# Kernel optimization log

Measured on AMD Instinct MI355X. Metric: run time of the kernel, lower is better.

The kernel has to match this reference:

```python
import jax, jax.numpy as jnp
import numpy as np

EPS = 1e-5

def _ln(x, g):
    # LayerNorm over the 3H gate dimension, scale-only (haste LayerNormGRU style)
    m = jnp.mean(x, axis=-1, keepdims=True)
    v = jnp.var(x, axis=-1, keepdims=True)
    return (x - m) * jax.lax.rsqrt(v + EPS) * g

def _gru_layer(x, h0, W, R, bx, br, gw, gr):
    # x: [B,T,D], h0: [B,H]; returns ([B,T,H], [B,H])
    H = R.shape[0]
    wx = _ln(jnp.einsum('btd,dk->btk', x, W), gw)  # [B,T,3H], LN precomputable (no h dep)

    def step(h, wx_t):
        rh = _ln(h @ R, gr)  # [B,3H]
        z = jax.nn.sigmoid(wx_t[:, :H] + bx[:H] + rh[:, :H] + br[:H])
        r = jax.nn.sigmoid(wx_t[:, H:2*H] + bx[H:2*H] + rh[:, H:2*H] + br[H:2*H])
        g = jnp.tanh(wx_t[:, 2*H:] + bx[2*H:] + r * (rh[:, 2*H:] + br[2*H:]))
        h_new = z * h + (1.0 - z) * g
        return h_new, h_new

    h_last, hs = jax.lax.scan(step, h0, jnp.swapaxes(wx, 0, 1))  # scan over T
    return jnp.swapaxes(hs, 0, 1), h_last

def setup_inputs() -> dict:
    key = jax.random.key(0)
    ks = jax.random.split(key, 8)
    B, T, IN, H, OUT, L = 32, 512, 128, 1024, 80, 3
    s_in = 1.0 / np.sqrt(IN)
    s_h = 1.0 / np.sqrt(H)
    return {
        'x': jax.random.normal(ks[0], (B, T, IN), jnp.float32),
        'W0': jax.random.normal(ks[1], (IN, 3 * H), jnp.float32) * s_in,
        'R0': jax.random.normal(ks[2], (H, 3 * H), jnp.float32) * s_h,
        'bx0': jnp.zeros((3 * H,), jnp.float32),
        'br0': jnp.zeros((3 * H,), jnp.float32),
        'gw0': jnp.ones((3 * H,), jnp.float32),
        'gr0': jnp.ones((3 * H,), jnp.float32),
        'Wk': jax.random.normal(ks[3], (L - 1, H, 3 * H), jnp.float32) * s_h,
        'Rk': jax.random.normal(ks[4], (L - 1, H, 3 * H), jnp.float32) * s_h,
        'bxk': jnp.zeros((L - 1, 3 * H), jnp.float32),
        'brk': jnp.zeros((L - 1, 3 * H), jnp.float32),
        'gwk': jnp.ones((L - 1, 3 * H), jnp.float32),
        'grk': jnp.ones((L - 1, 3 * H), jnp.float32),
        'Wlin': jax.random.normal(ks[5], (H, OUT), jnp.float32) * s_h,
        'blin': jnp.zeros((OUT,), jnp.float32),
    }

def reference(x, W0, R0, bx0, br0, gw0, gr0, Wk, Rk, bxk, brk, gwk, grk, Wlin, blin):
    B = x.shape[0]
    H = R0.shape[0]
    h0 = jnp.zeros((B, H), x.dtype)
    h, hs = _gru_layer(x, h0, W0, R0, bx0, br0, gw0, gr0)
    for i in range(Wk.shape[0]):  # stacked layers share state chain (state=h_s)
        h, hs = _gru_layer(h, hs, Wk[i], Rk[i], bxk[i], brk[i], gwk[i], grk[i])
    return jnp.tanh(h @ Wlin + blin)
```

## Files before the change

### kernel.cpp

```cpp
#include <hip/hip_runtime.h>


typedef float    f32x4 __attribute__((ext_vector_type(4)));
typedef _Float16 f16x8 __attribute__((ext_vector_type(8)));

#define HH      1024
#define TT      512
#define BBATCH  32
#define H3      3072
#define MROWS   16384
#define NBLK_R  128
#define HPB     8
#define COLS    24
#define LN_EPS  1e-5f

#define OFF_CTRL   0u
#define OFF_PSTAT  8192u
#define OFF_H      40960u
#define OFF_HF     106496u
#define CTRL_BYTES 237568u
#define OFF_WLB    327680u
#define OFF_WB     524288u
#define OFF_XBF    (8ull<<20)
#define OFF_WX     (16ull<<20)
#define OFF_HSA    (112ull<<20)
#define OFF_HSB    (144ull<<20)

#define ALOAD(p)    __hip_atomic_load((p),  __ATOMIC_RELAXED, __HIP_MEMORY_SCOPE_AGENT)
#define ASTORE(p,v) __hip_atomic_store((p), (v), __ATOMIC_RELAXED, __HIP_MEMORY_SCOPE_AGENT)
#define AADD(p)     __hip_atomic_fetch_add((p), 1u, __ATOMIC_RELAXED, __HIP_MEMORY_SCOPE_AGENT)

__device__ __forceinline__ f16x8 ldg_h16(const _Float16* p) {
  f16x8 r;
  asm volatile("global_load_dwordx4 %0, %1, off sc0 sc1" : "=v"(r) : "v"(p));
  return r;
}
__device__ __forceinline__ f32x4 ldg_f32x4(const float* p) {
  f32x4 r;
  asm volatile("global_load_dwordx4 %0, %1, off sc0 sc1" : "=v"(r) : "v"(p));
  return r;
}

__device__ __forceinline__ float sigf(float x) {
  return __builtin_amdgcn_rcpf(1.f + __expf(-x));
}
__device__ __forceinline__ float tanhfast(float x) {
  const float e2 = __expf(2.f * x);
  return 1.f - 2.f * __builtin_amdgcn_rcpf(e2 + 1.f);
}

__global__ __launch_bounds__(256, 1) void k_init(
    const float* __restrict__ x, _Float16* __restrict__ xb,
    const float* __restrict__ Wlin, _Float16* __restrict__ Wlb)
{
  const size_t stride = (size_t)gridDim.x * 256;
  for (size_t i = (size_t)blockIdx.x * 256 + threadIdx.x; i < (size_t)MROWS * 128; i += stride)
    xb[i] = (_Float16)x[i];
  for (size_t i = (size_t)blockIdx.x * 256 + threadIdx.x; i < 80u * 1024u; i += stride) {
    const size_t n = i >> 10, k = i & 1023u;
    Wlb[i] = (_Float16)Wlin[k * 80 + n];
  }
}

__global__ __launch_bounds__(256, 1) void k_convW(
    const float* __restrict__ W, _Float16* __restrict__ Wb, const int K)
{
  const int n = blockIdx.x;
  for (int k = threadIdx.x; k < K; k += 256)
    Wb[(size_t)n * K + k] = (_Float16)W[(size_t)k * H3 + n];
}

__global__ __launch_bounds__(256, 1) void k_gemm(
    const _Float16* __restrict__ A,
    const _Float16* __restrict__ Bw,
    _Float16* __restrict__ Cw,
    const int K)
{
  __shared__ _Float16 Bs[64][40];
  const int tid = threadIdx.x;
  const int lane = tid & 63, wv = tid >> 6;
  const int l15 = lane & 15, quad = lane >> 4;
  const int tilem = blockIdx.x / 48, tilen = blockIdx.x % 48;
  const int mbase = tilem * 64 + wv * 16;
  const size_t nbase = (size_t)tilen * 64;
  f32x4 acc[4] = {{0.f,0.f,0.f,0.f},{0.f,0.f,0.f,0.f},{0.f,0.f,0.f,0.f},{0.f,0.f,0.f,0.f}};
  const _Float16* arow = A + (size_t)(mbase + l15) * K + quad * 8;
  const int sn = tid >> 2, sk = (tid & 3) * 8;
  const _Float16* bsrc = Bw + (nbase + sn) * K + sk;
  for (int kc = 0; kc < K; kc += 32) {
    __syncthreads();
    *(f16x8*)(&Bs[sn][sk]) = *(const f16x8*)(bsrc + kc);
    __syncthreads();
    const f16x8 af = *(const f16x8*)(arow + kc);
#pragma unroll
    for (int nt = 0; nt < 4; ++nt) {
      const f16x8 bv = *(const f16x8*)(&Bs[nt * 16 + l15][quad * 8]);
      acc[nt] = __builtin_amdgcn_mfma_f32_16x16x32_f16(af, bv, acc[nt], 0, 0, 0);
    }
  }
#pragma unroll
  for (int nt = 0; nt < 4; ++nt)
#pragma unroll
    for (int j = 0; j < 4; ++j)
      Cw[(size_t)(mbase + quad * 4 + j) * H3 + nbase + nt * 16 + l15] = (_Float16)acc[nt][j];
}

__global__ __launch_bounds__(256, 1) void k_ln(
    _Float16* __restrict__ wxp, const float* __restrict__ gw)
{
  const int wv = threadIdx.x >> 6, lane = threadIdx.x & 63;
  const size_t row = (size_t)blockIdx.x * 4 + wv;
  _Float16* p = wxp + row * H3 + lane * 8;
  float vals[48];
  float s = 0.f, q = 0.f;
#pragma unroll
  for (int c = 0; c < 6; ++c) {
    const f16x8 v = *(const f16x8*)(p + c * 512);
#pragma unroll
    for (int j = 0; j < 8; ++j) {
      const float f = (float)v[j];
      vals[c * 8 + j] = f; s += f; q += f * f;
    }
  }
#pragma unroll
  for (int m = 1; m < 64; m <<= 1) { s += __shfl_xor(s, m); q += __shfl_xor(q, m); }
  const float mean = s * (1.f / H3);
  const float var  = q * (1.f / H3) - mean * mean;
  const float inv  = rsqrtf(var + LN_EPS);
#pragma unroll
  for (int c = 0; c < 6; ++c) {
    f16x8 o;
#pragma unroll
    for (int j = 0; j < 8; ++j)
      o[j] = (_Float16)((vals[c * 8 + j] - mean) * inv * gw[c * 512 + lane * 8 + j]);
    *(f16x8*)(p + c * 512) = o;
  }
}

__global__ __launch_bounds__(256, 1) void k_recur(
    const float* __restrict__ R, const float* __restrict__ bx,
    const float* __restrict__ br, const float* __restrict__ gr,
    const _Float16* __restrict__ wx,
    _Float16* __restrict__ hs_out,
    unsigned* __restrict__ hglob,
    float* __restrict__ hf32,
    float* __restrict__ pstat,
    unsigned* __restrict__ ctrl,
    const unsigned abase,
    const unsigned hbase)
{
  const int tid = threadIdx.x;
  const int blk = blockIdx.x;
  unsigned* cntA = ctrl;
  unsigned* cntB = ctrl + 1024;

  __shared__ _Float16 Rs[COLS][HH + 8];
  __shared__ float rhp[2][BBATCH][27];
  __shared__ float statb[BBATCH][2];
  __shared__ float pred[16][68];

  const int lane = tid & 63;
  const int wv   = tid >> 6;
  const int mh   = wv >> 1;
  const int kh   = wv & 1;
  const int l15  = lane & 15;
  const int quad = lane >> 4;
  const int kb   = kh * 512;
  const int lineB = ((blk & 7) * 4 + wv) * 32;

  for (int n = 0; n < COLS; ++n) {
    const int gc = (n >> 3) * HH + blk * HPB + (n & 7);
    for (int k = tid; k < HH; k += 256)
      Rs[n][k] = (_Float16)R[(size_t)k * H3 + gc];
  }

  const int b_row = tid >> 3;
  const int jj    = tid & 7;
  const int gi    = blk * HPB + jj;
  const float bxz = bx[gi], bxr = bx[HH + gi], bxg = bx[2 * HH + gi];
  const float brz = br[gi], brr = br[HH + gi], brg = br[2 * HH + gi];
  const float grz = gr[gi], grr = gr[HH + gi], grg = gr[2 * HH + gi];
  float hloc = hf32[b_row * HH + gi];

  {
    union { _Float16 f; unsigned short s; } hc; hc.f = (_Float16)hloc;
    const unsigned short mybits = hc.s;
    const unsigned short pbits  = (unsigned short)__shfl_xor((int)mybits, 1);
    if ((jj & 1) == 0) {
      const unsigned w = (unsigned)mybits | ((unsigned)pbits << 16);
      ASTORE(&hglob[blk * 128 + b_row * 4 + (jj >> 1)], w);
    }
  }
  asm volatile("s_waitcnt vmcnt(0)" ::: "memory");
  if (lane == 0) AADD(&cntB[lineB]);

  const _Float16* hread = (const _Float16*)hglob;
  const _Float16* hrow  = hread + (size_t)(kh * 64 + quad) * 256
                                + (size_t)(mh * 16 + l15) * 8;
  const int n1 = 16 + (l15 & 7);

  for (int t = 0; t < TT; ++t) {
    const _Float16* wrow = wx + (size_t)(b_row * TT + t) * H3;
    const float wz = (float)wrow[gi];
    const float wr = (float)wrow[HH + gi];
    const float wg = (float)wrow[2 * HH + gi];

    if (tid < 32) {
      const unsigned* p = cntB + tid * 32;
      const unsigned tgt = 16u * (hbase + (unsigned)t + 1u);
      int spins = 0;
      while (ALOAD(p) < tgt) { if (++spins > (1 << 24)) break; }
    }
    __syncthreads();

    f16x8 af[16];
#pragma unroll
    for (int ks = 0; ks < 16; ++ks)
      af[ks] = ldg_h16(hrow + ks * 1024);
    asm volatile("s_waitcnt vmcnt(0)" ::: "memory");
    f32x4 acc0 = {0.f,0.f,0.f,0.f}, acc1 = {0.f,0.f,0.f,0.f};
#pragma unroll
    for (int ks = 0; ks < 16; ++ks) {
      const f16x8 b0 = *(const f16x8*)(&Rs[l15][kb + ks * 32 + quad * 8]);
      acc0 = __builtin_amdgcn_mfma_f32_16x16x32_f16(af[ks], b0, acc0, 0, 0, 0);
      const f16x8 b1 = *(const f16x8*)(&Rs[n1][kb + ks * 32 + quad * 8]);
      acc1 = __builtin_amdgcn_mfma_f32_16x16x32_f16(af[ks], b1, acc1, 0, 0, 0);
    }
#pragma unroll
    for (int j = 0; j < 4; ++j) {
      rhp[kh][mh * 16 + quad * 4 + j][l15] = acc0[j];
      if (l15 < 8) rhp[kh][mh * 16 + quad * 4 + j][16 + l15] = acc1[j];
    }
    __syncthreads();

    const float rz = rhp[0][b_row][jj]      + rhp[1][b_row][jj];
    const float rr = rhp[0][b_row][8 + jj]  + rhp[1][b_row][8 + jj];
    const float rg = rhp[0][b_row][16 + jj] + rhp[1][b_row][16 + jj];
    {
      float s = rz + rr + rg;
      float q = rz * rz + rr * rr + rg * rg;
      s += __shfl_xor(s, 1); q += __shfl_xor(q, 1);
      s += __shfl_xor(s, 2); q += __shfl_xor(q, 2);
      s += __shfl_xor(s, 4); q += __shfl_xor(q, 4);
      if (jj == 0) { statb[b_row][0] = s; statb[b_row][1] = q; }
    }
    __syncthreads();
    if (tid < 64) ASTORE(&pstat[blk * 64 + tid], statb[tid >> 1][tid & 1]);
    asm volatile("s_waitcnt vmcnt(0)" ::: "memory");
    if (tid == 0) AADD(&cntA[(blk & 31) * 32]);

    if (tid < 32) {
      const unsigned* p = cntA + tid * 32;
      const unsigned tgt = 4u * (abase + (unsigned)t + 1u);
      int spins = 0;
      while (ALOAD(p) < tgt) { if (++spins > (1 << 24)) break; }
    }
    __syncthreads();

    {
      const int prow0 = tid >> 4;
      const int pcol  = (tid & 15) * 4;
      f32x4 pv0 = ldg_f32x4(pstat + (size_t)(prow0      ) * 64 + pcol);
      f32x4 pv1 = ldg_f32x4(pstat + (size_t)(prow0 +  16) * 64 + pcol);
      f32x4 pv2 = ldg_f32x4(pstat + (size_t)(prow0 +  32) * 64 + pcol);
      f32x4 pv3 = ldg_f32x4(pstat + (size_t)(prow0 +  48) * 64 + pcol);
      f32x4 pv4 = ldg_f32x4(pstat + (size_t)(prow0 +  64) * 64 + pcol);
      f32x4 pv5 = ldg_f32x4(pstat + (size_t)(prow0 +  80) * 64 + pcol);
      f32x4 pv6 = ldg_f32x4(pstat + (size_t)(prow0 +  96) * 64 + pcol);
      f32x4 pv7 = ldg_f32x4(pstat + (size_t)(prow0 + 112) * 64 + pcol);
      asm volatile("s_waitcnt vmcnt(0)" ::: "memory");
      const f32x4 pa = ((pv0 + pv1) + (pv2 + pv3)) + ((pv4 + pv5) + (pv6 + pv7));
      *(f32x4*)(&pred[prow0][pcol]) = pa;
    }
    __syncthreads();
    float sfs = 0.f, sfq = 0.f;
#pragma unroll
    for (int g = 0; g < 16; ++g) {
      sfs += pred[g][2 * b_row];
      sfq += pred[g][2 * b_row + 1];
    }

    const float mean = sfs * (1.f / H3);
    const float var  = sfq * (1.f / H3) - mean * mean;
    const float inv  = __frsqrt_rn(var + LN_EPS);
    const float rzn = (rz - mean) * inv * grz;
    const float rrn = (rr - mean) * inv * grr;
    const float rgn = (rg - mean) * inv * grg;
    const float zg    = sigf(wz + bxz + rzn + brz);
    const float rgate = sigf(wr + bxr + rrn + brr);
    const float gg    = tanhfast(wg + bxg + rgate * (rgn + brg));
    const float hn = zg * hloc + (1.f - zg) * gg;
    hloc = hn;
    union { _Float16 f; unsigned short s; } hc; hc.f = (_Float16)hn;
    const unsigned short mybits = hc.s;
    const unsigned short pbits  = (unsigned short)__shfl_xor((int)mybits, 1);
    if ((jj & 1) == 0) {
      const unsigned w = (unsigned)mybits | ((unsigned)pbits << 16);
      ASTORE(&hglob[blk * 128 + b_row * 4 + (jj >> 1)], w);
    }
    hs_out[(size_t)(b_row * TT + t) * HH + gi] = hc.f;
    asm volatile("s_waitcnt vmcnt(0)" ::: "memory");
    if (lane == 0) AADD(&cntB[lineB]);
  }
  hf32[b_row * HH + gi] = hloc;
}

__global__ __launch_bounds__(256, 1) void k_proj(
    const _Float16* __restrict__ hs,
    const _Float16* __restrict__ Wlb,
    const float* __restrict__ blin,
    float* __restrict__ out)
{
  const int tid = threadIdx.x, lane = tid & 63, wv = tid >> 6;
  const int l15 = lane & 15, quad = lane >> 4;
  const int mbase = blockIdx.x * 64 + wv * 16;
  f32x4 acc[5] = {{0.f,0.f,0.f,0.f},{0.f,0.f,0.f,0.f},{0.f,0.f,0.f,0.f},
                  {0.f,0.f,0.f,0.f},{0.f,0.f,0.f,0.f}};
  const _Float16* arow = hs + (size_t)(mbase + l15) * HH + quad * 8;
  for (int kc = 0; kc < HH; kc += 32) {
    const f16x8 af = *(const f16x8*)(arow + kc);
#pragma unroll
    for (int nt = 0; nt < 5; ++nt) {
      const f16x8 bv = *(const f16x8*)(Wlb + (size_t)(nt * 16 + l15) * HH + kc + quad * 8);
      acc[nt] = __builtin_amdgcn_mfma_f32_16x16x32_f16(af, bv, acc[nt], 0, 0, 0);
    }
  }
#pragma unroll
  for (int nt = 0; nt < 5; ++nt)
#pragma unroll
    for (int j = 0; j < 4; ++j) {
      const int col = nt * 16 + l15;
      out[(size_t)(mbase + quad * 4 + j) * 80 + col] = tanhf(acc[nt][j] + blin[col]);
    }
}

extern "C" void kernel_launch(void* const* d_in, const int* in_sizes, int n_in,
                              void* d_out, int out_size, void* d_ws, size_t ws_size,
                              hipStream_t stream)
{
  const float* x    = (const float*)d_in[0];
  const float* W0   = (const float*)d_in[1];
  const float* R0   = (const float*)d_in[2];
  const float* bx0  = (const float*)d_in[3];
  const float* br0  = (const float*)d_in[4];
  const float* gw0  = (const float*)d_in[5];
  const float* gr0  = (const float*)d_in[6];
  const float* Wk   = (const float*)d_in[7];
  const float* Rk   = (const float*)d_in[8];
  const float* bxk  = (const float*)d_in[9];
  const float* brk  = (const float*)d_in[10];
  const float* gwk  = (const float*)d_in[11];
  const float* grk  = (const float*)d_in[12];
  const float* Wlin = (const float*)d_in[13];
  const float* blin = (const float*)d_in[14];

  char* ws = (char*)d_ws;
  unsigned*  ctrl   = (unsigned*)(ws + OFF_CTRL);
  float*     pstat  = (float*)(ws + OFF_PSTAT);
  unsigned*  hglob  = (unsigned*)(ws + OFF_H);
  float*     hf32   = (float*)(ws + OFF_HF);
  _Float16*  Wlb    = (_Float16*)(ws + OFF_WLB);
  _Float16*  Wb     = (_Float16*)(ws + OFF_WB);
  _Float16*  xb     = (_Float16*)(ws + OFF_XBF);
  _Float16*  wx     = (_Float16*)(ws + OFF_WX);
  _Float16*  hsA    = (_Float16*)(ws + OFF_HSA);
  _Float16*  hsB    = (_Float16*)(ws + OFF_HSB);

  hipMemsetAsync(d_ws, 0, CTRL_BYTES, stream);

  k_init<<<2048, 256, 0, stream>>>(x, xb, Wlin, Wlb);

  for (int l = 0; l < 3; ++l) {
    const int K = l ? HH : 128;
    const float* Wl  = l ? (Wk  + (size_t)(l - 1) * HH * H3) : W0;
    const float* Rl  = l ? (Rk  + (size_t)(l - 1) * HH * H3) : R0;
    const float* bxl = l ? (bxk + (size_t)(l - 1) * H3) : bx0;
    const float* brl = l ? (brk + (size_t)(l - 1) * H3) : br0;
    const float* gwl = l ? (gwk + (size_t)(l - 1) * H3) : gw0;
    const float* grl = l ? (grk + (size_t)(l - 1) * H3) : gr0;
    const _Float16* Ain = (l == 0) ? xb : ((l == 1) ? hsA : hsB);
    _Float16* hs_out = (l == 1) ? hsB : hsA;

    k_convW<<<H3, 256, 0, stream>>>(Wl, Wb, K);
    k_gemm<<<12288, 256, 0, stream>>>(Ain, Wb, wx, K);
    k_ln<<<4096, 256, 0, stream>>>(wx, gwl);
    k_recur<<<NBLK_R, 256, 0, stream>>>(Rl, bxl, brl, grl, wx, hs_out,
                                        hglob, hf32, pstat, ctrl,
                                        (unsigned)l * (unsigned)TT,
                                        (unsigned)l * (TT + 1u));
  }
  k_proj<<<256, 256, 0, stream>>>(hsA, Wlb, blin, (float*)d_out);
}
```

Baseline: 10.68 ms.

## Replace counter barrier for LN stats with tagged data polling

Removes the cntA atomic-counter barrier used to exchange per-block LayerNorm partial sums across the 128 recurrent blocks. Each block now writes its sum and sum-of-squares together with a timestep tag in one 16-byte store, and readers spin on the tag embedded in the data itself. This saves a store-wait-atomic-poll round trip on every timestep. It relies on 16-byte stores being seen whole and on float tags staying exact, and all 256 threads now poll global memory.

```diff
diff --git a/kernel.cpp b/kernel.cpp
--- a/kernel.cpp
+++ b/kernel.cpp
@@ -15,10 +15,10 @@
 #define LN_EPS  1e-5f
 
 #define OFF_CTRL   0u
-#define OFF_PSTAT  8192u
-#define OFF_H      40960u
-#define OFF_HF     106496u
-#define CTRL_BYTES 237568u
+#define OFF_PST    4096u
+#define OFF_H      69632u
+#define OFF_HF     135168u
+#define CTRL_BYTES 266240u
 #define OFF_WLB    327680u
 #define OFF_WB     524288u
 #define OFF_XBF    (8ull<<20)
@@ -39,6 +39,9 @@
   f32x4 r;
   asm volatile("global_load_dwordx4 %0, %1, off sc0 sc1" : "=v"(r) : "v"(p));
   return r;
+}
+__device__ __forceinline__ void stg_f32x4(float* p, f32x4 v) {
+  asm volatile("global_store_dwordx4 %0, %1, off sc0 sc1" :: "v"(p), "v"(v) : "memory");
 }
 
 __device__ __forceinline__ float sigf(float x) {
@@ -144,20 +147,20 @@
     _Float16* __restrict__ hs_out,
     unsigned* __restrict__ hglob,
     float* __restrict__ hf32,
-    float* __restrict__ pstat,
+    float* __restrict__ pst,
     unsigned* __restrict__ ctrl,
     const unsigned abase,
     const unsigned hbase)
 {
   const int tid = threadIdx.x;
   const int blk = blockIdx.x;
-  unsigned* cntA = ctrl;
-  unsigned* cntB = ctrl + 1024;
+  unsigned* cntB = ctrl;
 
   __shared__ _Float16 Rs[COLS][HH + 8];
   __shared__ float rhp[2][BBATCH][27];
   __shared__ float statb[BBATCH][2];
-  __shared__ float pred[16][68];
+  __shared__ float predS[8][33];
+  __shared__ float predQ[8][33];
 
   const int lane = tid & 63;
   const int wv   = tid >> 6;
@@ -198,8 +201,12 @@
   const _Float16* hrow  = hread + (size_t)(kh * 64 + quad) * 256
                                 + (size_t)(mh * 16 + l15) * 8;
   const int n1 = 16 + (l15 & 7);
+  const int grp = tid >> 5;
+  const int rr  = tid & 31;
+  const float* gbase = pst + ((size_t)(grp * 16) * 32 + rr) * 4;
 
   for (int t = 0; t < TT; ++t) {
+    const float tagf = (float)(abase + (unsigned)t + 1u);
     const _Float16* wrow = wx + (size_t)(b_row * TT + t) * H3;
     const float wz = (float)wrow[gi];
     const float wr = (float)wrow[HH + gi];
@@ -234,57 +241,57 @@
     __syncthreads();
 
     const float rz = rhp[0][b_row][jj]      + rhp[1][b_row][jj];
-    const float rr = rhp[0][b_row][8 + jj]  + rhp[1][b_row][8 + jj];
+    const float rr2 = rhp[0][b_row][8 + jj]  + rhp[1][b_row][8 + jj];
     const float rg = rhp[0][b_row][16 + jj] + rhp[1][b_row][16 + jj];
     {
-      float s = rz + rr + rg;
-      float q = rz * rz + rr * rr + rg * rg;
+      float s = rz + rr2 + rg;
+      float q = rz * rz + rr2 * rr2 + rg * rg;
       s += __shfl_xor(s, 1); q += __shfl_xor(q, 1);
       s += __shfl_xor(s, 2); q += __shfl_xor(q, 2);
       s += __shfl_xor(s, 4); q += __shfl_xor(q, 4);
       if (jj == 0) { statb[b_row][0] = s; statb[b_row][1] = q; }
     }
     __syncthreads();
-    if (tid < 64) ASTORE(&pstat[blk * 64 + tid], statb[tid >> 1][tid & 1]);
-    asm volatile("s_waitcnt vmcnt(0)" ::: "memory");
-    if (tid == 0) AADD(&cntA[(blk & 31) * 32]);
 
     if (tid < 32) {
-      const unsigned* p = cntA + tid * 32;
-      const unsigned tgt = 4u * (abase + (unsigned)t + 1u);
-      int spins = 0;
-      while (ALOAD(p) < tgt) { if (++spins > (1 << 24)) break; }
-    }
-    __syncthreads();
+      f32x4 pv;
+      pv[0] = statb[tid][0]; pv[1] = tagf;
+      pv[2] = statb[tid][1]; pv[3] = tagf;
+      stg_f32x4(pst + ((size_t)blk * 32 + tid) * 4, pv);
+    }
 
     {
-      const int prow0 = tid >> 4;
-      const int pcol  = (tid & 15) * 4;
-      f32x4 pv0 = ldg_f32x4(pstat + (size_t)(prow0      ) * 64 + pcol);
-      f32x4 pv1 = ldg_f32x4(pstat + (size_t)(prow0 +  16) * 64 + pcol);
-      f32x4 pv2 = ldg_f32x4(pstat + (size_t)(prow0 +  32) * 64 + pcol);
-      f32x4 pv3 = ldg_f32x4(pstat + (size_t)(prow0 +  48) * 64 + pcol);
-      f32x4 pv4 = ldg_f32x4(pstat + (size_t)(prow0 +  64) * 64 + pcol);
-      f32x4 pv5 = ldg_f32x4(pstat + (size_t)(prow0 +  80) * 64 + pcol);
-      f32x4 pv6 = ldg_f32x4(pstat + (size_t)(prow0 +  96) * 64 + pcol);
-      f32x4 pv7 = ldg_f32x4(pstat + (size_t)(prow0 + 112) * 64 + pcol);
+      f32x4 pv[16];
+#pragma unroll
+      for (int i = 0; i < 16; ++i) pv[i] = ldg_f32x4(gbase + i * 128);
       asm volatile("s_waitcnt vmcnt(0)" ::: "memory");
-      const f32x4 pa = ((pv0 + pv1) + (pv2 + pv3)) + ((pv4 + pv5) + (pv6 + pv7));
-      *(f32x4*)(&pred[prow0][pcol]) = pa;
+      float ss = 0.f, qq = 0.f;
+#pragma unroll
+      for (int i = 0; i < 16; ++i) {
+        f32x4 v = pv[i];
+        int spins = 0;
+        while (v[1] != tagf || v[3] != tagf) {
+          v = ldg_f32x4(gbase + i * 128);
+          asm volatile("s_waitcnt vmcnt(0)" ::: "memory");
+          if (++spins > (1 << 22)) break;
+        }
+        ss += v[0]; qq += v[2];
+      }
+      predS[grp][rr] = ss; predQ[grp][rr] = qq;
     }
     __syncthreads();
     float sfs = 0.f, sfq = 0.f;
 #pragma unroll
-    for (int g = 0; g < 16; ++g) {
-      sfs += pred[g][2 * b_row];
-      sfq += pred[g][2 * b_row + 1];
+    for (int g = 0; g < 8; ++g) {
+      sfs += predS[g][b_row];
+      sfq += predQ[g][b_row];
     }
 
     const float mean = sfs * (1.f / H3);
     const float var  = sfq * (1.f / H3) - mean * mean;
     const float inv  = __frsqrt_rn(var + LN_EPS);
     const float rzn = (rz - mean) * inv * grz;
-    const float rrn = (rr - mean) * inv * grr;
+    const float rrn = (rr2 - mean) * inv * grr;
     const float rgn = (rg - mean) * inv * grg;
     const float zg    = sigf(wz + bxz + rzn + brz);
     const float rgate = sigf(wr + bxr + rrn + brr);
@@ -356,7 +363,7 @@
 
   char* ws = (char*)d_ws;
   unsigned*  ctrl   = (unsigned*)(ws + OFF_CTRL);
-  float*     pstat  = (float*)(ws + OFF_PSTAT);
+  float*     pst    = (float*)(ws + OFF_PST);
   unsigned*  hglob  = (unsigned*)(ws + OFF_H);
   float*     hf32   = (float*)(ws + OFF_HF);
   _Float16*  Wlb    = (_Float16*)(ws + OFF_WLB);
@@ -385,7 +392,7 @@
     k_gemm<<<12288, 256, 0, stream>>>(Ain, Wb, wx, K);
     k_ln<<<4096, 256, 0, stream>>>(wx, gwl);
     k_recur<<<NBLK_R, 256, 0, stream>>>(Rl, bxl, brl, grl, wx, hs_out,
-                                        hglob, hf32, pstat, ctrl,
+                                        hglob, hf32, pst, ctrl,
                                         (unsigned)l * (unsigned)TT,
                                         (unsigned)l * (TT + 1u));
   }
```

Result: slower. 16.70 ms (+56.3%).
